# Performance work log

Hardware: AMD Instinct MI355X
Metric: run time of the kernel (lower is better)

The kernel has to match this reference:

```python
import jax, jax.numpy as jnp
import numpy as np

N_USER = 8192
N_PRODUCT = 8192
E = 128
D = 64
K = 32
M = 4


def _make_nbrs(m, n, k, n_other, salt):
    # distinct neighbor indices per (metapath, node): step = n_other // k guarantees
    # the k offsets are distinct modulo n_other (matches set-like ragged lists)
    i = np.arange(m)[:, None, None]
    j = np.arange(n)[None, :, None]
    t = np.arange(k)[None, None, :]
    idx = (j * 7 + i * 131 + salt * 17 + t * (n_other // k)) % n_other
    return jnp.asarray(idx, dtype=jnp.int32)


def setup_inputs() -> dict:
    key = jax.random.key(0)
    ks = jax.random.split(key, 16)
    s = 0.1
    return {
        "user": jax.random.normal(ks[0], (N_USER, E), jnp.float32),
        "product": jax.random.normal(ks[1], (N_PRODUCT, E), jnp.float32),
        "V": jax.random.normal(ks[2], (2, M, E, D), jnp.float32) * s,
        "X": jax.random.normal(ks[3], (2, M, 1, D), jnp.float32) * s,
        "W_p": jax.random.normal(ks[4], (2, M, E, D), jnp.float32) * s,
        "B_p": jax.random.normal(ks[5], (2, M, D), jnp.float32) * s,
        "W_q": jax.random.normal(ks[6], (2, M, E, D), jnp.float32) * s,
        "B_q": jax.random.normal(ks[7], (2, M, D), jnp.float32) * s,
        "Q": jax.random.normal(ks[8], (2, M, 1, D), jnp.float32) * s,
        "user_nbrs": _make_nbrs(M, N_USER, K, N_PRODUCT, 0),
        "product_nbrs": _make_nbrs(M, N_PRODUCT, K, N_USER, 1),
    }


def _phase(src, other, nbrs, v, x, w, b, wq, bq, q):
    # src: [n,E], other: [n_other,E], nbrs: [M,n,K] indices into other
    m, n, k = nbrs.shape
    n_other = other.shape[0]
    nbr_emb = other[nbrs]  # [M,n,K,E] ragged gather
    proj_src = jnp.einsum('ne,med->mnd', src, v)          # [M,n,D]
    proj_nbr = jnp.einsum('mnke,med->mnkd', nbr_emb, w)   # [M,n,K,D]
    h = jnp.tanh(proj_src[:, :, None, :] + proj_nbr + b[:, None, None, :])
    scores = jnp.einsum('mnkd,md->mnk', h, x[:, 0])       # [M,n,K]
    # Faithful to torch: non-neighbor logit is -1e-9 for metapath 0; for
    # metapath i>=1 the repeated whole-tensor softmax makes it 1/n_other.
    baseline = jnp.where(jnp.arange(m) == 0,
                         jnp.float32(-1e-9),
                         jnp.float32(1.0) / n_other)      # [M]
    mx = jnp.maximum(scores.max(-1), baseline[:, None])   # [M,n]
    e = jnp.exp(scores - mx[..., None])
    denom = e.sum(-1) + (n_other - k) * jnp.exp(baseline[:, None] - mx)
    A = e / denom[..., None]                              # softmax over full axis
    # H aggregation uses detached attention weights (A.data in torch)
    H = src[None] + jnp.einsum('mnk,mnke->mne', jax.lax.stop_gradient(A), nbr_emb)
    sem = jnp.tanh(jnp.einsum('mne,med->mnd', H, wq) + bq[:, None, :])
    beta_raw = jax.lax.stop_gradient(
        jnp.einsum('mnd,md->mn', sem, q[:, 0]).mean(-1))  # [M], detached (.data)
    beta = jax.nn.softmax(beta_raw)
    return jnp.einsum('m,mne->ne', beta, H)


def reference(user, product, V, X, W_p, B_p, W_q, B_q, Q, user_nbrs, product_nbrs):
    user_out = _phase(user, product, user_nbrs,
                      V[0], X[0], W_p[0], B_p[0], W_q[0], B_q[0], Q[0])
    # product phase attends over the UPDATED user embeddings
    product_out = _phase(product, user_out, product_nbrs,
                         V[1], X[1], W_p[1], B_p[1], W_q[1], B_q[1], Q[1])
    return (user_out, product_out)
```

## Files before the change

kernel.cpp:

```cpp
#include <hip/hip_runtime.h>
#include <hip/hip_bf16.h>

#define NN 8192
#define ED 128
#define DD 64
#define KK 32
#define MM 4

typedef __attribute__((ext_vector_type(8))) short short8;
typedef __attribute__((ext_vector_type(4))) float f32x4;

__device__ __forceinline__ float ftanh(float x)
{
    const float e = __expf(2.0f * x);
    return fmaf(-2.0f, __builtin_amdgcn_rcpf(e + 1.0f), 1.0f);
}

__device__ __forceinline__ unsigned short f2bf(float x)
{
    __hip_bfloat16 b = __float2bfloat16(x);
    return *reinterpret_cast<unsigned short*>(&b);
}
__device__ __forceinline__ float bflo(unsigned int u) { return __uint_as_float(u << 16); }
__device__ __forceinline__ float bfhi(unsigned int u) { return __uint_as_float(u & 0xFFFF0000u); }
__device__ __forceinline__ float readlane_f(float v, int lane)
{
    return __uint_as_float(__builtin_amdgcn_readlane(__float_as_uint(v), lane));
}

__global__ __launch_bounds__(256) void convert2_kernel(
    const float* __restrict__ inA, unsigned short* __restrict__ outA,
    const float* __restrict__ inB, unsigned short* __restrict__ outB)
{
    const float* in = blockIdx.y ? inB : inA;
    unsigned short* out = blockIdx.y ? outB : outA;
    const int i = blockIdx.x * 256 + threadIdx.x;
    const float4 v = ((const float4*)in)[i];
    uint2 o;
    o.x = (unsigned int)f2bf(v.x) | ((unsigned int)f2bf(v.y) << 16);
    o.y = (unsigned int)f2bf(v.z) | ((unsigned int)f2bf(v.w) << 16);
    ((uint2*)out)[i] = o;
}

__global__ __launch_bounds__(256) void transpose3_kernel(
    const float* __restrict__ inV, unsigned short* __restrict__ outV,
    const float* __restrict__ inP, unsigned short* __restrict__ outP,
    const float* __restrict__ inQ, unsigned short* __restrict__ outQ)
{
    const float* in = (blockIdx.y == 0) ? inV : (blockIdx.y == 1) ? inP : inQ;
    unsigned short* out = (blockIdx.y == 0) ? outV : (blockIdx.y == 1) ? outP : outQ;
    const int gid = blockIdx.x * 256 + threadIdx.x;
    const int s   = gid >> 13;
    const int rem = gid & 8191;
    const int e   = rem >> 6;
    const int d   = rem & 63;
    out[((size_t)s * DD + d) * ED + e] = f2bf(in[gid]);
}

__global__ __launch_bounds__(256) void proj2_mfma(
    const unsigned short* __restrict__ emb0,
    const unsigned short* __restrict__ Wt0,
    const float* __restrict__ Bias0,
    float* __restrict__ outF0,
    const unsigned short* __restrict__ emb1,
    const unsigned short* __restrict__ Wt1,
    unsigned short* __restrict__ outB1)
{
    const int z    = blockIdx.z;
    const int m    = blockIdx.y;
    const int tid  = threadIdx.x;
    const int wave = tid >> 6;
    const int lane = tid & 63;
    const int nrow = lane & 15;
    const int quad = lane >> 4;
    const int r0   = blockIdx.x * 64 + wave * 16;

    const unsigned short* embB = z ? emb1 : emb0;
    const unsigned short* WtB  = z ? Wt1 : Wt0;

    const short8* A8 = (const short8*)(embB + (size_t)(r0 + nrow) * ED);
    const short8* B8 = (const short8*)(WtB + (size_t)m * DD * ED);

    f32x4 acc0 = {0.f, 0.f, 0.f, 0.f};
    f32x4 acc1 = {0.f, 0.f, 0.f, 0.f};
    f32x4 acc2 = {0.f, 0.f, 0.f, 0.f};
    f32x4 acc3 = {0.f, 0.f, 0.f, 0.f};

    #pragma unroll
    for (int kq = 0; kq < 4; ++kq) {
        const short8 a = A8[kq * 4 + quad];
        const short8 b0 = B8[(0 * 16 + nrow) * 16 + kq * 4 + quad];
        const short8 b1 = B8[(1 * 16 + nrow) * 16 + kq * 4 + quad];
        const short8 b2 = B8[(2 * 16 + nrow) * 16 + kq * 4 + quad];
        const short8 b3 = B8[(3 * 16 + nrow) * 16 + kq * 4 + quad];
        acc0 = __builtin_amdgcn_mfma_f32_16x16x32_bf16(a, b0, acc0, 0, 0, 0);
        acc1 = __builtin_amdgcn_mfma_f32_16x16x32_bf16(a, b1, acc1, 0, 0, 0);
        acc2 = __builtin_amdgcn_mfma_f32_16x16x32_bf16(a, b2, acc2, 0, 0, 0);
        acc3 = __builtin_amdgcn_mfma_f32_16x16x32_bf16(a, b3, acc3, 0, 0, 0);
    }

    f32x4 accs[4] = {acc0, acc1, acc2, acc3};
    if (z == 0) {
        #pragma unroll
        for (int t = 0; t < 4; ++t) {
            const int d = t * 16 + nrow;
            const float bv = Bias0[m * DD + d];
            #pragma unroll
            for (int reg = 0; reg < 4; ++reg) {
                const int r = r0 + quad * 4 + reg;
                outF0[((size_t)m * NN + r) * DD + d] = accs[t][reg] + bv;
            }
        }
    } else {
        #pragma unroll
        for (int t = 0; t < 4; ++t) {
            const int d = t * 16 + nrow;
            #pragma unroll
            for (int reg = 0; reg < 4; ++reg) {
                const int r = r0 + quad * 4 + reg;
                outB1[((size_t)m * NN + r) * DD + d] = f2bf(accs[t][reg]);
            }
        }
    }
}

__global__ __launch_bounds__(256) void attn_kernel(
    const float* __restrict__ src,
    const unsigned short* __restrict__ otherB,
    const int*   __restrict__ nbrs,
    const float* __restrict__ S,
    const unsigned short* __restrict__ PnB,
    const float* __restrict__ Xv,
    unsigned short* __restrict__ HoutB)
{
    const int m    = blockIdx.y;
    const int tid  = threadIdx.x;
    const int w    = tid >> 6;
    const int lane = tid & 63;
    const int j    = blockIdx.x * 4 + w;

    const int kg = lane >> 4;
    const int dq = lane & 15;

    int idxreg = 0;
    if (lane < KK) idxreg = nbrs[((size_t)m * NN + j) * KK + lane];

    const float4 S4 = *(const float4*)(S + ((size_t)m * NN + j) * DD + dq * 4);
    const float4 X4 = *(const float4*)(Xv + (size_t)m * DD + dq * 4);

    float e_arr[8];
    #pragma unroll
    for (int i = 0; i < 8; ++i) {
        const int jk = __shfl(idxreg, i * 4 + kg, 64);
        const uint2 pv = ((const uint2*)(PnB + ((size_t)m * NN + jk) * DD))[dq];
        float p = ftanh(S4.x + bflo(pv.x)) * X4.x;
        p = fmaf(ftanh(S4.y + bfhi(pv.x)), X4.y, p);
        p = fmaf(ftanh(S4.z + bflo(pv.y)), X4.z, p);
        p = fmaf(ftanh(S4.w + bfhi(pv.y)), X4.w, p);
        p += __shfl_xor(p, 1, 64);
        p += __shfl_xor(p, 2, 64);
        p += __shfl_xor(p, 4, 64);
        p += __shfl_xor(p, 8, 64);
        e_arr[i] = p;
    }

    const float baseline = (m == 0) ? -1e-9f : (1.0f / (float)NN);
    float mx = e_arr[0];
    #pragma unroll
    for (int i = 1; i < 8; ++i) mx = fmaxf(mx, e_arr[i]);
    mx = fmaxf(mx, __shfl_xor(mx, 16, 64));
    mx = fmaxf(mx, __shfl_xor(mx, 32, 64));
    mx = fmaxf(mx, baseline);
    float sum = 0.0f;
    #pragma unroll
    for (int i = 0; i < 8; ++i) { e_arr[i] = __expf(e_arr[i] - mx); sum += e_arr[i]; }
    sum += __shfl_xor(sum, 16, 64);
    sum += __shfl_xor(sum, 32, 64);
    const float inv_denom =
        __builtin_amdgcn_rcpf(sum + (float)(NN - KK) * __expf(baseline - mx));
    #pragma unroll
    for (int i = 0; i < 8; ++i) e_arr[i] *= inv_denom;

    float2 h = ((const float2*)(src + (size_t)j * ED))[lane];
    #pragma unroll
    for (int k = 0; k < KK; ++k) {
        const float a  = readlane_f(e_arr[k >> 2], (k & 3) * 16);
        const int   jk = __builtin_amdgcn_readlane(idxreg, k);
        const unsigned int ov = ((const unsigned int*)(otherB + (size_t)jk * ED))[lane];
        h.x = fmaf(a, bflo(ov), h.x);
        h.y = fmaf(a, bfhi(ov), h.y);
    }
    const unsigned int hu =
        (unsigned int)f2bf(h.x) | ((unsigned int)f2bf(h.y) << 16);
    ((unsigned int*)(HoutB + ((size_t)m * NN + j) * ED))[lane] = hu;
}

__global__ __launch_bounds__(256) void sem_mfma(
    const unsigned short* __restrict__ HB,
    const unsigned short* __restrict__ WqT,
    const float* __restrict__ Bq,
    const float* __restrict__ Qv,
    float* __restrict__ bp)
{
    const int m    = blockIdx.y;
    const int tid  = threadIdx.x;
    const int wave = tid >> 6;
    const int lane = tid & 63;
    const int nrow = lane & 15;
    const int quad = lane >> 4;
    const int r0   = blockIdx.x * 64 + wave * 16;

    __shared__ float red_sh[4];

    const short8* A8 = (const short8*)(HB + ((size_t)m * NN + r0 + nrow) * ED);
    const short8* B8 = (const short8*)(WqT + (size_t)m * DD * ED);

    f32x4 acc0 = {0.f, 0.f, 0.f, 0.f};
    f32x4 acc1 = {0.f, 0.f, 0.f, 0.f};
    f32x4 acc2 = {0.f, 0.f, 0.f, 0.f};
    f32x4 acc3 = {0.f, 0.f, 0.f, 0.f};

    #pragma unroll
    for (int kq = 0; kq < 4; ++kq) {
        const short8 a = A8[kq * 4 + quad];
        const short8 b0 = B8[(0 * 16 + nrow) * 16 + kq * 4 + quad];
        const short8 b1 = B8[(1 * 16 + nrow) * 16 + kq * 4 + quad];
        const short8 b2 = B8[(2 * 16 + nrow) * 16 + kq * 4 + quad];
        const short8 b3 = B8[(3 * 16 + nrow) * 16 + kq * 4 + quad];
        acc0 = __builtin_amdgcn_mfma_f32_16x16x32_bf16(a, b0, acc0, 0, 0, 0);
        acc1 = __builtin_amdgcn_mfma_f32_16x16x32_bf16(a, b1, acc1, 0, 0, 0);
        acc2 = __builtin_amdgcn_mfma_f32_16x16x32_bf16(a, b2, acc2, 0, 0, 0);
        acc3 = __builtin_amdgcn_mfma_f32_16x16x32_bf16(a, b3, acc3, 0, 0, 0);
    }

    f32x4 accs[4] = {acc0, acc1, acc2, acc3};
    float part = 0.0f;
    #pragma unroll
    for (int t = 0; t < 4; ++t) {
        const int d = t * 16 + nrow;
        const float bq = Bq[m * DD + d];
        const float qv = Qv[m * DD + d];
        #pragma unroll
        for (int reg = 0; reg < 4; ++reg)
            part = fmaf(ftanh(accs[t][reg] + bq), qv, part);
    }
    #pragma unroll
    for (int off = 32; off; off >>= 1) part += __shfl_xor(part, off, 64);
    if (lane == 0) red_sh[wave] = part;
    __syncthreads();
    if (tid == 0)
        bp[m * 128 + blockIdx.x] =
            (red_sh[0] + red_sh[1]) + (red_sh[2] + red_sh[3]);
}

__global__ void beta_reduce(const float* __restrict__ bp, float* __restrict__ bw)
{
    const int lane = threadIdx.x;
    const int m = lane >> 4, t = lane & 15;
    float s = 0.0f;
    #pragma unroll
    for (int i = 0; i < 8; ++i)
        s += bp[m * 128 + t + i * 16];
    s += __shfl_xor(s, 1, 64);
    s += __shfl_xor(s, 2, 64);
    s += __shfl_xor(s, 4, 64);
    s += __shfl_xor(s, 8, 64);
    const float v = s * (1.0f / (float)NN);
    float mx = v;
    mx = fmaxf(mx, __shfl_xor(mx, 16, 64));
    mx = fmaxf(mx, __shfl_xor(mx, 32, 64));
    const float e = expf(v - mx);
    float es = e;
    es += __shfl_xor(es, 16, 64);
    es += __shfl_xor(es, 32, 64);
    if (t == 0) bw[m] = e / es;
}

__global__ __launch_bounds__(256) void combine_kernel(
    const unsigned short* __restrict__ HB,
    const float* __restrict__ bw,
    float* __restrict__ outp,
    unsigned short* __restrict__ outB)
{
    const int i = blockIdx.x * 256 + threadIdx.x;
    const size_t st = (size_t)NN * ED / 4;
    const uint2* h = (const uint2*)HB;
    float r0 = 0.f, r1 = 0.f, r2 = 0.f, r3 = 0.f;
    #pragma unroll
    for (int s = 0; s < MM; ++s) {
        const float b = bw[s];
        const uint2 v = h[s * st + i];
        r0 = fmaf(b, bflo(v.x), r0);
        r1 = fmaf(b, bfhi(v.x), r1);
        r2 = fmaf(b, bflo(v.y), r2);
        r3 = fmaf(b, bfhi(v.y), r3);
    }
    float4 o; o.x = r0; o.y = r1; o.z = r2; o.w = r3;
    ((float4*)outp)[i] = o;
    if (outB) {
        uint2 ob;
        ob.x = (unsigned int)f2bf(r0) | ((unsigned int)f2bf(r1) << 16);
        ob.y = (unsigned int)f2bf(r2) | ((unsigned int)f2bf(r3) << 16);
        ((uint2*)outB)[i] = ob;
    }
}

extern "C" void kernel_launch(void* const* d_in, const int* in_sizes, int n_in,
                              void* d_out, int out_size, void* d_ws, size_t ws_size,
                              hipStream_t stream)
{
    const float* user    = (const float*)d_in[0];
    const float* product = (const float*)d_in[1];
    const float* V   = (const float*)d_in[2];
    const float* X   = (const float*)d_in[3];
    const float* W_p = (const float*)d_in[4];
    const float* B_p = (const float*)d_in[5];
    const float* W_q = (const float*)d_in[6];
    const float* B_q = (const float*)d_in[7];
    const float* Q   = (const float*)d_in[8];
    const int* user_nbrs    = (const int*)d_in[9];
    const int* product_nbrs = (const int*)d_in[10];

    float* out  = (float*)d_out;
    float* out0 = out;
    float* out1 = out + (size_t)NN * ED;

    float* ws = (float*)d_ws;
    float* bp = ws;
    float* bw = bp + 1024;
    float* S  = bw + 16;
    unsigned short* us = (unsigned short*)(S + (size_t)MM * NN * DD);
    unsigned short* PnB      = us;
    unsigned short* HB       = PnB + (size_t)MM * NN * DD;
    unsigned short* userB    = HB + (size_t)MM * NN * ED;
    unsigned short* productB = userB + (size_t)NN * ED;
    unsigned short* oB       = productB + (size_t)NN * ED;
    unsigned short* VT       = oB + (size_t)NN * ED;
    unsigned short* PT       = VT + (size_t)2 * MM * DD * ED;
    unsigned short* QT       = PT + (size_t)2 * MM * DD * ED;

    const size_t MED = (size_t)MM * ED * DD;
    const size_t MD  = (size_t)MM * DD;

    const dim3 gM2(NN / 64, MM, 2);
    const dim3 gM(NN / 64, MM);
    const dim3 gA(NN / 4, MM);
    const int cBlocks = (NN * ED / 4) / 256;
    const int wN = 2 * MM * ED * DD;

    convert2_kernel<<<dim3(cBlocks, 2), 256, 0, stream>>>(user, userB,
                                                          product, productB);
    transpose3_kernel<<<dim3(wN / 256, 3), 256, 0, stream>>>(V, VT, W_p, PT,
                                                             W_q, QT);

    {
        proj2_mfma<<<gM2, 256, 0, stream>>>(userB, VT, B_p, S,
                                            productB, PT, PnB);
        attn_kernel<<<gA, 256, 0, stream>>>(user, productB, user_nbrs,
                                            S, PnB, X, HB);
        sem_mfma<<<gM, 256, 0, stream>>>(HB, QT, B_q, Q, bp);
        beta_reduce<<<1, 64, 0, stream>>>(bp, bw);
        combine_kernel<<<cBlocks, 256, 0, stream>>>(HB, bw, out0, oB);
    }

    {
        proj2_mfma<<<gM2, 256, 0, stream>>>(productB, VT + MED, B_p + MD, S,
                                            oB, PT + MED, PnB);
        attn_kernel<<<gA, 256, 0, stream>>>(product, oB, product_nbrs,
                                            S, PnB, X + MD, HB);
        sem_mfma<<<gM, 256, 0, stream>>>(HB, QT + MED, B_q + MD, Q + MD, bp);
        beta_reduce<<<1, 64, 0, stream>>>(bp, bw);
        combine_kernel<<<cBlocks, 256, 0, stream>>>(HB, bw, out1, nullptr);
    }
}
```

Measured before the change: 210.3 us.

## Merge prep kernels, fold beta reduce into combine, two nodes per wave in attention

Three changes. The bf16 conversion and weight transpose kernels merge into one launch. The beta softmax reduction moves into every combine block, which drops a one-block launch and the workspace buffer it wrote. The attention kernel now handles two destination nodes per wave, interleaving their gathers to raise memory-level parallelism, at the cost of more registers and half as many blocks.

```diff
diff --git a/kernel.cpp b/kernel.cpp
--- a/kernel.cpp
+++ b/kernel.cpp
@@ -28,33 +28,34 @@
     return __uint_as_float(__builtin_amdgcn_readlane(__float_as_uint(v), lane));
 }
 
-__global__ __launch_bounds__(256) void convert2_kernel(
-    const float* __restrict__ inA, unsigned short* __restrict__ outA,
-    const float* __restrict__ inB, unsigned short* __restrict__ outB)
-{
-    const float* in = blockIdx.y ? inB : inA;
-    unsigned short* out = blockIdx.y ? outB : outA;
-    const int i = blockIdx.x * 256 + threadIdx.x;
-    const float4 v = ((const float4*)in)[i];
-    uint2 o;
-    o.x = (unsigned int)f2bf(v.x) | ((unsigned int)f2bf(v.y) << 16);
-    o.y = (unsigned int)f2bf(v.z) | ((unsigned int)f2bf(v.w) << 16);
-    ((uint2*)out)[i] = o;
-}
-
-__global__ __launch_bounds__(256) void transpose3_kernel(
-    const float* __restrict__ inV, unsigned short* __restrict__ outV,
-    const float* __restrict__ inP, unsigned short* __restrict__ outP,
-    const float* __restrict__ inQ, unsigned short* __restrict__ outQ)
-{
-    const float* in = (blockIdx.y == 0) ? inV : (blockIdx.y == 1) ? inP : inQ;
-    unsigned short* out = (blockIdx.y == 0) ? outV : (blockIdx.y == 1) ? outP : outQ;
-    const int gid = blockIdx.x * 256 + threadIdx.x;
-    const int s   = gid >> 13;
-    const int rem = gid & 8191;
-    const int e   = rem >> 6;
-    const int d   = rem & 63;
-    out[((size_t)s * DD + d) * ED + e] = f2bf(in[gid]);
+__global__ __launch_bounds__(256) void prep_kernel(
+    const float* __restrict__ user, unsigned short* __restrict__ userB,
+    const float* __restrict__ product, unsigned short* __restrict__ productB,
+    const float* __restrict__ V, unsigned short* __restrict__ VT,
+    const float* __restrict__ Wp, unsigned short* __restrict__ PT,
+    const float* __restrict__ Wq, unsigned short* __restrict__ QT)
+{
+    const int y = blockIdx.y;
+    if (y < 2) {
+        const float* in = y ? product : user;
+        unsigned short* out = y ? productB : userB;
+        const int i = blockIdx.x * 256 + threadIdx.x;
+        const float4 v = ((const float4*)in)[i];
+        uint2 o;
+        o.x = (unsigned int)f2bf(v.x) | ((unsigned int)f2bf(v.y) << 16);
+        o.y = (unsigned int)f2bf(v.z) | ((unsigned int)f2bf(v.w) << 16);
+        ((uint2*)out)[i] = o;
+    } else {
+        if (blockIdx.x >= 256) return;
+        const float* in = (y == 2) ? V : (y == 3) ? Wp : Wq;
+        unsigned short* out = (y == 2) ? VT : (y == 3) ? PT : QT;
+        const int gid = blockIdx.x * 256 + threadIdx.x;
+        const int s   = gid >> 13;
+        const int rem = gid & 8191;
+        const int e   = rem >> 6;
+        const int d   = rem & 63;
+        out[((size_t)s * DD + d) * ED + e] = f2bf(in[gid]);
+    }
 }
 
 __global__ __launch_bounds__(256) void proj2_mfma(
@@ -137,62 +138,91 @@
     const int tid  = threadIdx.x;
     const int w    = tid >> 6;
     const int lane = tid & 63;
-    const int j    = blockIdx.x * 4 + w;
+    const int g    = blockIdx.x * 4 + w;
+    const int j0   = g * 2;
+    const int j1   = g * 2 + 1;
 
     const int kg = lane >> 4;
     const int dq = lane & 15;
 
-    int idxreg = 0;
-    if (lane < KK) idxreg = nbrs[((size_t)m * NN + j) * KK + lane];
-
-    const float4 S4 = *(const float4*)(S + ((size_t)m * NN + j) * DD + dq * 4);
-    const float4 X4 = *(const float4*)(Xv + (size_t)m * DD + dq * 4);
-
-    float e_arr[8];
+    const int jj = (lane < 32) ? j0 : j1;
+    const int idxreg = nbrs[((size_t)m * NN + jj) * KK + (lane & 31)];
+
+    const float4 S40 = *(const float4*)(S + ((size_t)m * NN + j0) * DD + dq * 4);
+    const float4 S41 = *(const float4*)(S + ((size_t)m * NN + j1) * DD + dq * 4);
+    const float4 X4  = *(const float4*)(Xv + (size_t)m * DD + dq * 4);
+    const float2 hs0 = ((const float2*)(src + (size_t)j0 * ED))[lane];
+    const float2 hs1 = ((const float2*)(src + (size_t)j1 * ED))[lane];
+
+    float ea0[8], ea1[8];
     #pragma unroll
     for (int i = 0; i < 8; ++i) {
-        const int jk = __shfl(idxreg, i * 4 + kg, 64);
-        const uint2 pv = ((const uint2*)(PnB + ((size_t)m * NN + jk) * DD))[dq];
-        float p = ftanh(S4.x + bflo(pv.x)) * X4.x;
-        p = fmaf(ftanh(S4.y + bfhi(pv.x)), X4.y, p);
-        p = fmaf(ftanh(S4.z + bflo(pv.y)), X4.z, p);
-        p = fmaf(ftanh(S4.w + bfhi(pv.y)), X4.w, p);
-        p += __shfl_xor(p, 1, 64);
-        p += __shfl_xor(p, 2, 64);
-        p += __shfl_xor(p, 4, 64);
-        p += __shfl_xor(p, 8, 64);
-        e_arr[i] = p;
+        const int k  = i * 4 + kg;
+        const int jk0 = __shfl(idxreg, k, 64);
+        const int jk1 = __shfl(idxreg, 32 + k, 64);
+        const uint2 pv0 = ((const uint2*)(PnB + ((size_t)m * NN + jk0) * DD))[dq];
+        const uint2 pv1 = ((const uint2*)(PnB + ((size_t)m * NN + jk1) * DD))[dq];
+        float p0 = ftanh(S40.x + bflo(pv0.x)) * X4.x;
+        float p1 = ftanh(S41.x + bflo(pv1.x)) * X4.x;
+        p0 = fmaf(ftanh(S40.y + bfhi(pv0.x)), X4.y, p0);
+        p1 = fmaf(ftanh(S41.y + bfhi(pv1.x)), X4.y, p1);
+        p0 = fmaf(ftanh(S40.z + bflo(pv0.y)), X4.z, p0);
+        p1 = fmaf(ftanh(S41.z + bflo(pv1.y)), X4.z, p1);
+        p0 = fmaf(ftanh(S40.w + bfhi(pv0.y)), X4.w, p0);
+        p1 = fmaf(ftanh(S41.w + bfhi(pv1.y)), X4.w, p1);
+        p0 += __shfl_xor(p0, 1, 64);  p1 += __shfl_xor(p1, 1, 64);
+        p0 += __shfl_xor(p0, 2, 64);  p1 += __shfl_xor(p1, 2, 64);
+        p0 += __shfl_xor(p0, 4, 64);  p1 += __shfl_xor(p1, 4, 64);
+        p0 += __shfl_xor(p0, 8, 64);  p1 += __shfl_xor(p1, 8, 64);
+        ea0[i] = p0;
+        ea1[i] = p1;
     }
 
     const float baseline = (m == 0) ? -1e-9f : (1.0f / (float)NN);
-    float mx = e_arr[0];
-    #pragma unroll
-    for (int i = 1; i < 8; ++i) mx = fmaxf(mx, e_arr[i]);
-    mx = fmaxf(mx, __shfl_xor(mx, 16, 64));
-    mx = fmaxf(mx, __shfl_xor(mx, 32, 64));
-    mx = fmaxf(mx, baseline);
-    float sum = 0.0f;
-    #pragma unroll
-    for (int i = 0; i < 8; ++i) { e_arr[i] = __expf(e_arr[i] - mx); sum += e_arr[i]; }
-    sum += __shfl_xor(sum, 16, 64);
-    sum += __shfl_xor(sum, 32, 64);
-    const float inv_denom =
-        __builtin_amdgcn_rcpf(sum + (float)(NN - KK) * __expf(baseline - mx));
-    #pragma unroll
-    for (int i = 0; i < 8; ++i) e_arr[i] *= inv_denom;
-
-    float2 h = ((const float2*)(src + (size_t)j * ED))[lane];
+    float mx0 = ea0[0], mx1 = ea1[0];
+    #pragma unroll
+    for (int i = 1; i < 8; ++i) { mx0 = fmaxf(mx0, ea0[i]); mx1 = fmaxf(mx1, ea1[i]); }
+    mx0 = fmaxf(mx0, __shfl_xor(mx0, 16, 64));
+    mx1 = fmaxf(mx1, __shfl_xor(mx1, 16, 64));
+    mx0 = fmaxf(mx0, __shfl_xor(mx0, 32, 64));
+    mx1 = fmaxf(mx1, __shfl_xor(mx1, 32, 64));
+    mx0 = fmaxf(mx0, baseline);
+    mx1 = fmaxf(mx1, baseline);
+    float sum0 = 0.0f, sum1 = 0.0f;
+    #pragma unroll
+    for (int i = 0; i < 8; ++i) {
+        ea0[i] = __expf(ea0[i] - mx0); sum0 += ea0[i];
+        ea1[i] = __expf(ea1[i] - mx1); sum1 += ea1[i];
+    }
+    sum0 += __shfl_xor(sum0, 16, 64);  sum1 += __shfl_xor(sum1, 16, 64);
+    sum0 += __shfl_xor(sum0, 32, 64);  sum1 += __shfl_xor(sum1, 32, 64);
+    const float inv0 =
+        __builtin_amdgcn_rcpf(sum0 + (float)(NN - KK) * __expf(baseline - mx0));
+    const float inv1 =
+        __builtin_amdgcn_rcpf(sum1 + (float)(NN - KK) * __expf(baseline - mx1));
+    #pragma unroll
+    for (int i = 0; i < 8; ++i) { ea0[i] *= inv0; ea1[i] *= inv1; }
+
+    float2 ha = hs0, hb = hs1;
     #pragma unroll
     for (int k = 0; k < KK; ++k) {
-        const float a  = readlane_f(e_arr[k >> 2], (k & 3) * 16);
-        const int   jk = __builtin_amdgcn_readlane(idxreg, k);
-        const unsigned int ov = ((const unsigned int*)(otherB + (size_t)jk * ED))[lane];
-        h.x = fmaf(a, bflo(ov), h.x);
-        h.y = fmaf(a, bfhi(ov), h.y);
-    }
-    const unsigned int hu =
-        (unsigned int)f2bf(h.x) | ((unsigned int)f2bf(h.y) << 16);
-    ((unsigned int*)(HoutB + ((size_t)m * NN + j) * ED))[lane] = hu;
+        const float a0 = readlane_f(ea0[k >> 2], (k & 3) * 16);
+        const float a1 = readlane_f(ea1[k >> 2], (k & 3) * 16);
+        const int  jk0 = __builtin_amdgcn_readlane(idxreg, k);
+        const int  jk1 = __builtin_amdgcn_readlane(idxreg, 32 + k);
+        const unsigned int o0 = ((const unsigned int*)(otherB + (size_t)jk0 * ED))[lane];
+        const unsigned int o1 = ((const unsigned int*)(otherB + (size_t)jk1 * ED))[lane];
+        ha.x = fmaf(a0, bflo(o0), ha.x);
+        hb.x = fmaf(a1, bflo(o1), hb.x);
+        ha.y = fmaf(a0, bfhi(o0), ha.y);
+        hb.y = fmaf(a1, bfhi(o1), hb.y);
+    }
+    const unsigned int hu0 =
+        (unsigned int)f2bf(ha.x) | ((unsigned int)f2bf(ha.y) << 16);
+    const unsigned int hu1 =
+        (unsigned int)f2bf(hb.x) | ((unsigned int)f2bf(hb.y) << 16);
+    ((unsigned int*)(HoutB + ((size_t)m * NN + j0) * ED))[lane] = hu0;
+    ((unsigned int*)(HoutB + ((size_t)m * NN + j1) * ED))[lane] = hu1;
 }
 
 __global__ __launch_bounds__(256) void sem_mfma(
@@ -253,42 +283,43 @@
             (red_sh[0] + red_sh[1]) + (red_sh[2] + red_sh[3]);
 }
 
-__global__ void beta_reduce(const float* __restrict__ bp, float* __restrict__ bw)
-{
-    const int lane = threadIdx.x;
-    const int m = lane >> 4, t = lane & 15;
-    float s = 0.0f;
-    #pragma unroll
-    for (int i = 0; i < 8; ++i)
-        s += bp[m * 128 + t + i * 16];
-    s += __shfl_xor(s, 1, 64);
-    s += __shfl_xor(s, 2, 64);
-    s += __shfl_xor(s, 4, 64);
-    s += __shfl_xor(s, 8, 64);
-    const float v = s * (1.0f / (float)NN);
-    float mx = v;
-    mx = fmaxf(mx, __shfl_xor(mx, 16, 64));
-    mx = fmaxf(mx, __shfl_xor(mx, 32, 64));
-    const float e = expf(v - mx);
-    float es = e;
-    es += __shfl_xor(es, 16, 64);
-    es += __shfl_xor(es, 32, 64);
-    if (t == 0) bw[m] = e / es;
-}
-
 __global__ __launch_bounds__(256) void combine_kernel(
     const unsigned short* __restrict__ HB,
-    const float* __restrict__ bw,
+    const float* __restrict__ bp,
     float* __restrict__ outp,
     unsigned short* __restrict__ outB)
 {
-    const int i = blockIdx.x * 256 + threadIdx.x;
+    __shared__ float bw_sh[4];
+    const int tid = threadIdx.x;
+    if (tid < 64) {
+        const int m = tid >> 4, t = tid & 15;
+        float s = 0.0f;
+        #pragma unroll
+        for (int i = 0; i < 8; ++i)
+            s += bp[m * 128 + t + i * 16];
+        s += __shfl_xor(s, 1, 64);
+        s += __shfl_xor(s, 2, 64);
+        s += __shfl_xor(s, 4, 64);
+        s += __shfl_xor(s, 8, 64);
+        const float v = s * (1.0f / (float)NN);
+        float mx = v;
+        mx = fmaxf(mx, __shfl_xor(mx, 16, 64));
+        mx = fmaxf(mx, __shfl_xor(mx, 32, 64));
+        const float e = expf(v - mx);
+        float es = e;
+        es += __shfl_xor(es, 16, 64);
+        es += __shfl_xor(es, 32, 64);
+        if (t == 0) bw_sh[m] = e / es;
+    }
+    __syncthreads();
+
+    const int i = blockIdx.x * 256 + tid;
     const size_t st = (size_t)NN * ED / 4;
     const uint2* h = (const uint2*)HB;
     float r0 = 0.f, r1 = 0.f, r2 = 0.f, r3 = 0.f;
     #pragma unroll
     for (int s = 0; s < MM; ++s) {
-        const float b = bw[s];
+        const float b = bw_sh[s];
         const uint2 v = h[s * st + i];
         r0 = fmaf(b, bflo(v.x), r0);
         r1 = fmaf(b, bfhi(v.x), r1);
@@ -327,8 +358,7 @@
 
     float* ws = (float*)d_ws;
     float* bp = ws;
-    float* bw = bp + 1024;
-    float* S  = bw + 16;
+    float* S  = bp + 1024;
     unsigned short* us = (unsigned short*)(S + (size_t)MM * NN * DD);
     unsigned short* PnB      = us;
     unsigned short* HB       = PnB + (size_t)MM * NN * DD;
@@ -344,14 +374,11 @@
 
     const dim3 gM2(NN / 64, MM, 2);
     const dim3 gM(NN / 64, MM);
-    const dim3 gA(NN / 4, MM);
+    const dim3 gA(NN / 8, MM);
     const int cBlocks = (NN * ED / 4) / 256;
-    const int wN = 2 * MM * ED * DD;
-
-    convert2_kernel<<<dim3(cBlocks, 2), 256, 0, stream>>>(user, userB,
-                                                          product, productB);
-    transpose3_kernel<<<dim3(wN / 256, 3), 256, 0, stream>>>(V, VT, W_p, PT,
-                                                             W_q, QT);
+
+    prep_kernel<<<dim3(1024, 5), 256, 0, stream>>>(user, userB, product, productB,
+                                                   V, VT, W_p, PT, W_q, QT);
 
     {
         proj2_mfma<<<gM2, 256, 0, stream>>>(userB, VT, B_p, S,
@@ -359,8 +386,7 @@
         attn_kernel<<<gA, 256, 0, stream>>>(user, productB, user_nbrs,
                                             S, PnB, X, HB);
         sem_mfma<<<gM, 256, 0, stream>>>(HB, QT, B_q, Q, bp);
-        beta_reduce<<<1, 64, 0, stream>>>(bp, bw);
-        combine_kernel<<<cBlocks, 256, 0, stream>>>(HB, bw, out0, oB);
+        combine_kernel<<<cBlocks, 256, 0, stream>>>(HB, bp, out0, oB);
     }
 
     {
@@ -369,7 +395,6 @@
         attn_kernel<<<gA, 256, 0, stream>>>(product, oB, product_nbrs,
                                             S, PnB, X + MD, HB);
         sem_mfma<<<gM, 256, 0, stream>>>(HB, QT + MED, B_q + MD, Q + MD, bp);
-        beta_reduce<<<1, 64, 0, stream>>>(bp, bw);
-        combine_kernel<<<cBlocks, 256, 0, stream>>>(HB, bw, out1, nullptr);
-    }
-}
+        combine_kernel<<<cBlocks, 256, 0, stream>>>(HB, bp, out1, nullptr);
+    }
+}
```

After: 209.3 us. Within noise of the previous version (-0.5%).
